# Kernel tuning notes

Hardware: AMD Instinct MI355X
Metric: run time of the kernel (lower is better)

## Reference

```python
import jax, jax.numpy as jnp
import numpy as np

STRIDE = 16
RATIOS = (0.5, 1.0, 2.0)
SCALES = (8, 16, 32)
NMS_THRESH = 0.7
NUM_PRE = 12000
NUM_POST = 2000
MIN_SIZE = 16.0


def _all_anchors(feat_h, feat_w):
    # base anchors centered at (stride/2, stride/2), (y1, x1, y2, x2)
    base = []
    for r in RATIOS:
        for s in SCALES:
            h = STRIDE * s * np.sqrt(r)
            w = STRIDE * s * np.sqrt(1.0 / r)
            c = STRIDE / 2.0
            base.append([c - h / 2.0, c - w / 2.0, c + h / 2.0, c + w / 2.0])
    base = np.asarray(base, np.float32)  # (A, 4)
    ys = np.arange(feat_h, dtype=np.float32) * STRIDE
    xs = np.arange(feat_w, dtype=np.float32) * STRIDE
    shift = np.stack(np.meshgrid(ys, xs, indexing='ij'), axis=-1)  # (H, W, 2) = (y, x)
    shift4 = np.concatenate([shift, shift], axis=-1)  # (H, W, 4)
    anchors = shift4[:, :, None, :] + base[None, None, :, :]  # (H, W, A, 4)
    return jnp.asarray(anchors.reshape(-1, 4))


def _conv(x, w, b, padding):
    y = jax.lax.conv_general_dilated(x, w, (1, 1), padding,
                                     dimension_numbers=('NCHW', 'OIHW', 'NCHW'))
    return y + b[None, :, None, None]


def _create_rpn_proposals(locs, scores, anchors, img_h, img_w):
    # box deparameterize (y1,x1,y2,x2 anchors; dy,dx,dh,dw locs)
    ha = anchors[:, 2] - anchors[:, 0]
    wa = anchors[:, 3] - anchors[:, 1]
    cya = anchors[:, 0] + 0.5 * ha
    cxa = anchors[:, 1] + 0.5 * wa
    cy = locs[:, 0] * ha + cya
    cx = locs[:, 1] * wa + cxa
    h = ha * jnp.exp(locs[:, 2])
    w = wa * jnp.exp(locs[:, 3])
    boxes = jnp.stack([cy - 0.5 * h, cx - 0.5 * w, cy + 0.5 * h, cx + 0.5 * w], axis=1)

    order = jnp.argsort(-scores)[:NUM_PRE]
    boxes = boxes[order]
    s = scores[order]

    lim = jnp.array([img_h, img_w, img_h, img_w], dtype=boxes.dtype)
    boxes = jnp.clip(boxes, 0.0, lim)
    valid = ((boxes[:, 2] - boxes[:, 0]) >= MIN_SIZE) & ((boxes[:, 3] - boxes[:, 1]) >= MIN_SIZE)

    areas = (boxes[:, 2] - boxes[:, 0]) * (boxes[:, 3] - boxes[:, 1])
    n = boxes.shape[0]
    idx = jnp.arange(n)

    def body(i, suppressed):
        bi = boxes[i]
        yy1 = jnp.maximum(bi[0], boxes[:, 0])
        xx1 = jnp.maximum(bi[1], boxes[:, 1])
        yy2 = jnp.minimum(bi[2], boxes[:, 2])
        xx2 = jnp.minimum(bi[3], boxes[:, 3])
        inter = jnp.maximum(yy2 - yy1, 0.0) * jnp.maximum(xx2 - xx1, 0.0)
        iou = inter / (areas[i] + areas - inter + 1e-10)
        new_sup = suppressed | ((iou > NMS_THRESH) & (idx > i))
        return jnp.where(suppressed[i], suppressed, new_sup)

    suppressed = jax.lax.fori_loop(0, n, body, ~valid)
    keep = (~suppressed) & valid
    rank = jnp.cumsum(keep) - 1
    tgt = jnp.where(keep & (rank < NUM_POST), rank, NUM_POST)  # overflow slot
    out = jnp.zeros((NUM_POST + 1, 4), boxes.dtype).at[tgt].set(boxes)[:NUM_POST]
    return out  # (2000, 4), zero-padded if fewer kept


def setup_inputs() -> dict:
    key = jax.random.key(0)
    ks = jax.random.split(key, 7)
    in_c, out_c, A = 1024, 512, 9
    x = jax.random.normal(ks[0], (1, in_c, 64, 64), dtype=jnp.float32)
    conv_w = jax.random.normal(ks[1], (out_c, in_c, 3, 3), jnp.float32) * 0.01
    conv_b = jnp.zeros((out_c,), jnp.float32)
    score_w = jax.random.normal(ks[2], (A * 2, out_c, 1, 1), jnp.float32) * 0.01
    score_b = jnp.zeros((A * 2,), jnp.float32)
    loc_w = jax.random.normal(ks[3], (A * 4, out_c, 1, 1), jnp.float32) * 0.01
    loc_b = jnp.zeros((A * 4,), jnp.float32)
    return {"x": x, "conv_w": conv_w, "conv_b": conv_b,
            "score_w": score_w, "score_b": score_b,
            "loc_w": loc_w, "loc_b": loc_b,
            "img_h": 1024, "img_w": 1024}


def reference(x, conv_w, conv_b, score_w, score_b, loc_w, loc_b, img_h, img_w):
    _, _, fh, fw = x.shape
    anchors = _all_anchors(fh, fw)  # (fh*fw*A, 4)
    h = jax.nn.leaky_relu(_conv(x, conv_w, conv_b, 'SAME'), 0.01)
    rpn_locs = _conv(h, loc_w, loc_b, 'VALID').transpose(0, 2, 3, 1).reshape(-1, 4)
    rpn_scores = _conv(h, score_w, score_b, 'VALID').transpose(0, 2, 3, 1).reshape(-1, 2)
    fg = jax.nn.softmax(rpn_scores, axis=1)[:, 1]
    rois = _create_rpn_proposals(jax.lax.stop_gradient(rpn_locs),
                                 jax.lax.stop_gradient(fg),
                                 anchors, img_h, img_w)
    return rpn_locs, rpn_scores, rois, anchors
```

## Files before the change

kernel.cpp:

```cpp
#include <hip/hip_runtime.h>
#include <cstdint>
#include <cstddef>
#include <math.h>

#define NANCH    36864
#define NPRE     12000
#define NPRE_PAD 12032
#define NW       188
#define SORT_N   16384
#define NPOST    2000

__device__ __forceinline__ int tribase(int ci) { return ci * NW - (ci * (ci - 1)) / 2; }

__global__ __launch_bounds__(256, 2)
void k_conv_ks(const float* __restrict__ xg, const float* __restrict__ wg_,
               double* __restrict__ p0g, double* __restrict__ p1g)
{
    __shared__ float wlds[144 * 64];
    __shared__ float xlds[16 * 4 * 76];
    const int tid = threadIdx.x;
    const int ks  = blockIdx.x >> 8;
    const int inner = blockIdx.x & 255;
    const int oct = inner & 7;
    const int rp  = inner >> 3;
    const int oc0 = oct << 6;
    const int y0  = rp << 1;
    const int ocg = tid >> 4;
    const int pxg = tid & 15;
    const int ry  = pxg >> 3;
    const int cx0 = (pxg & 7) << 3;
    const int lane = tid & 63, wv = tid >> 6;
    const int icbase = ks << 9;

    double acc[4][8];
#pragma unroll
    for (int o = 0; o < 4; ++o)
#pragma unroll
        for (int j = 0; j < 8; ++j) acc[o][j] = 0.0;

    int xoff[17], loff[17];
#pragma unroll
    for (int t = 0; t < 17; ++t) {
        int f = tid + 256 * t;
        if (f < 4224) {
            int ic = f / 264; int r = f - ic * 264; int srow = r / 66; int gc = r - srow * 66;
            loff[t] = (ic * 4 + srow) * 76 + gc;
            int gy = y0 + srow - 1, gx = gc - 1;
            xoff[t] = (gy >= 0 && gy < 64 && gx >= 0 && gx < 64)
                      ? (ic * 4096 + gy * 64 + gx) : -1;
        } else { loff[t] = -1; xoff[t] = -1; }
    }

    const float* wbase = wg_ + (size_t)(oc0 + lane) * 9216 + (size_t)icbase * 9 + wv;
    const float* xbase = xg + (size_t)icbase * 4096;
    float wreg[36], xreg[17];

#pragma unroll
    for (int t = 0; t < 36; ++t) wreg[t] = wbase[4 * t];
#pragma unroll
    for (int t = 0; t < 17; ++t) xreg[t] = (xoff[t] >= 0) ? xbase[xoff[t]] : 0.f;

    for (int kc = 0; kc < 32; ++kc) {
        __syncthreads();
#pragma unroll
        for (int t = 0; t < 36; ++t) wlds[(wv + 4 * t) * 64 + lane] = wreg[t];
#pragma unroll
        for (int t = 0; t < 17; ++t)
            if (loff[t] >= 0) xlds[loff[t]] = xreg[t];
        if (kc < 31) {
            const float* wp = wbase + (kc + 1) * 144;
            const float* xp = xbase + (size_t)(kc + 1) * 16 * 4096;
#pragma unroll
            for (int t = 0; t < 36; ++t) wreg[t] = wp[4 * t];
#pragma unroll
            for (int t = 0; t < 17; ++t) xreg[t] = (xoff[t] >= 0) ? xp[xoff[t]] : 0.f;
        }
        __syncthreads();
#pragma unroll 1
        for (int ic = 0; ic < 16; ++ic) {
#pragma unroll
            for (int ky = 0; ky < 3; ++ky) {
                const float* xr = &xlds[(ic * 4 + ry + ky) * 76 + cx0];
                float4 t0 = *(const float4*)(xr);
                float4 t1 = *(const float4*)(xr + 4);
                float2 t2 = *(const float2*)(xr + 8);
                double xwd[10] = {t0.x, t0.y, t0.z, t0.w, t1.x, t1.y, t1.z, t1.w, t2.x, t2.y};
#pragma unroll
                for (int kx = 0; kx < 3; ++kx) {
                    const float4 wq = *(const float4*)&wlds[(ic * 9 + ky * 3 + kx) * 64 + (ocg << 2)];
                    double wdv[4] = {wq.x, wq.y, wq.z, wq.w};
#pragma unroll
                    for (int o = 0; o < 4; ++o)
#pragma unroll
                        for (int j = 0; j < 8; ++j)
                            acc[o][j] = fma(wdv[o], xwd[j + kx], acc[o][j]);
                }
            }
        }
    }
    double* pg = ks ? p1g : p0g;
#pragma unroll
    for (int o = 0; o < 4; ++o) {
        const int oc = oc0 + (ocg << 2) + o;
        double* pp = pg + (size_t)oc * 4096 + (y0 + ry) * 64 + cx0;
#pragma unroll
        for (int j = 0; j < 8; j += 2)
            *(double2*)(pp + j) = make_double2(acc[o][j], acc[o][j + 1]);
    }
}

__global__ __launch_bounds__(256, 4)
void k_comb(const double* __restrict__ p0, const double* __restrict__ p1,
            const float* __restrict__ bg, float* __restrict__ hg)
{
    int i2 = (blockIdx.x * 256 + threadIdx.x) * 2;
    double2 a = *(const double2*)(p0 + i2);
    double2 b = *(const double2*)(p1 + i2);
    double bo = (double)bg[i2 >> 12];
    double t0 = a.x + b.x + bo, t1 = a.y + b.y + bo;
    float v0 = (float)((t0 >= 0.0) ? t0 : 0.01 * t0);
    float v1 = (float)((t1 >= 0.0) ? t1 : 0.01 * t1);
    *(float2*)(hg + i2) = make_float2(v0, v1);
}

__global__ __launch_bounds__(256, 1)
void k_conv_full(const float* __restrict__ xg, const float* __restrict__ wg_,
                 const float* __restrict__ bg, float* __restrict__ hg)
{
    __shared__ float wlds[144 * 64];
    __shared__ float xlds[16 * 4 * 76];
    const int tid = threadIdx.x;
    const int oct = blockIdx.x & 7;
    const int rp  = blockIdx.x >> 3;
    const int oc0 = oct << 6;
    const int y0  = rp << 1;
    const int ocg = tid >> 4;
    const int pxg = tid & 15;
    const int ry  = pxg >> 3;
    const int cx0 = (pxg & 7) << 3;
    const int lane = tid & 63, wv = tid >> 6;
    double acc[4][8];
#pragma unroll
    for (int o = 0; o < 4; ++o)
#pragma unroll
        for (int j = 0; j < 8; ++j) acc[o][j] = 0.0;
    int xoff[17], loff[17];
#pragma unroll
    for (int t = 0; t < 17; ++t) {
        int f = tid + 256 * t;
        if (f < 4224) {
            int ic = f / 264; int r = f - ic * 264; int srow = r / 66; int gc = r - srow * 66;
            loff[t] = (ic * 4 + srow) * 76 + gc;
            int gy = y0 + srow - 1, gx = gc - 1;
            xoff[t] = (gy >= 0 && gy < 64 && gx >= 0 && gx < 64)
                      ? (ic * 4096 + gy * 64 + gx) : -1;
        } else { loff[t] = -1; xoff[t] = -1; }
    }
    const float* wbase = wg_ + (size_t)(oc0 + lane) * 9216 + wv;
    float wreg[36], xreg[17];
#pragma unroll
    for (int t = 0; t < 36; ++t) wreg[t] = wbase[4 * t];
#pragma unroll
    for (int t = 0; t < 17; ++t) xreg[t] = (xoff[t] >= 0) ? xg[xoff[t]] : 0.f;
    for (int kc = 0; kc < 64; ++kc) {
        __syncthreads();
#pragma unroll
        for (int t = 0; t < 36; ++t) wlds[(wv + 4 * t) * 64 + lane] = wreg[t];
#pragma unroll
        for (int t = 0; t < 17; ++t)
            if (loff[t] >= 0) xlds[loff[t]] = xreg[t];
        if (kc < 63) {
            const float* wp = wbase + (kc + 1) * 144;
            const float* xp = xg + (size_t)(kc + 1) * 16 * 4096;
#pragma unroll
            for (int t = 0; t < 36; ++t) wreg[t] = wp[4 * t];
#pragma unroll
            for (int t = 0; t < 17; ++t) xreg[t] = (xoff[t] >= 0) ? xp[xoff[t]] : 0.f;
        }
        __syncthreads();
#pragma unroll 1
        for (int ic = 0; ic < 16; ++ic) {
#pragma unroll
            for (int ky = 0; ky < 3; ++ky) {
                const float* xr = &xlds[(ic * 4 + ry + ky) * 76 + cx0];
                float4 t0 = *(const float4*)(xr);
                float4 t1 = *(const float4*)(xr + 4);
                float2 t2 = *(const float2*)(xr + 8);
                double xwd[10] = {t0.x, t0.y, t0.z, t0.w, t1.x, t1.y, t1.z, t1.w, t2.x, t2.y};
#pragma unroll
                for (int kx = 0; kx < 3; ++kx) {
                    const float4 wq = *(const float4*)&wlds[(ic * 9 + ky * 3 + kx) * 64 + (ocg << 2)];
                    double wdv[4] = {wq.x, wq.y, wq.z, wq.w};
#pragma unroll
                    for (int o = 0; o < 4; ++o)
#pragma unroll
                        for (int j = 0; j < 8; ++j)
                            acc[o][j] = fma(wdv[o], xwd[j + kx], acc[o][j]);
                }
            }
        }
    }
#pragma unroll
    for (int o = 0; o < 4; ++o) {
        const int oc = oc0 + (ocg << 2) + o;
        const double bo = (double)bg[oc];
        float* hp = hg + (size_t)oc * 4096 + (y0 + ry) * 64 + cx0;
        float v[8];
#pragma unroll
        for (int j = 0; j < 8; ++j) {
            double t = acc[o][j] + bo;
            v[j] = (float)((t >= 0.0) ? t : 0.01 * t);
        }
        *(float4*)(hp)     = make_float4(v[0], v[1], v[2], v[3]);
        *(float4*)(hp + 4) = make_float4(v[4], v[5], v[6], v[7]);
    }
}

__global__ __launch_bounds__(256, 1)
void k_heads(const float* __restrict__ hg, const float* __restrict__ loc_w,
             const float* __restrict__ loc_b, const float* __restrict__ score_w,
             const float* __restrict__ score_b, const int* __restrict__ imh,
             const int* __restrict__ imw, float* __restrict__ out,
             float* __restrict__ boxes_all, unsigned long long* __restrict__ keys64)
{
    __shared__ float  hch[64 * 64];
    __shared__ float  wch[54 * 64];
    __shared__ float  ol[54 * 64];
    __shared__ double sld[18 * 64];
    const int y = blockIdx.x, tid = threadIdx.x;
    const int px = tid & 63, cg = tid >> 6;
    double acc[14];
#pragma unroll
    for (int u = 0; u < 14; ++u) acc[u] = 0.0;
    for (int cc = 0; cc < 8; ++cc) {
        __syncthreads();
#pragma unroll
        for (int t = 0; t < 16; ++t) {
            int f = tid + 256 * t;
            hch[f] = hg[(size_t)(cc * 64 + (f >> 6)) * 4096 + y * 64 + (f & 63)];
        }
#pragma unroll
        for (int t = 0; t < 14; ++t) {
            int f = tid + 256 * t;
            if (f < 54 * 64) {
                int ch = f >> 6, c = f & 63;
                wch[f] = (ch < 36) ? loc_w[ch * 512 + cc * 64 + c]
                                   : score_w[(ch - 36) * 512 + cc * 64 + c];
            }
        }
        __syncthreads();
        for (int c = 0; c < 64; ++c) {
            double hvd = (double)hch[c * 64 + px];
#pragma unroll
            for (int u = 0; u < 14; ++u) {
                int ch = cg + 4 * u;
                if (ch < 54) acc[u] = fma((double)wch[ch * 64 + c], hvd, acc[u]);
            }
        }
    }
    __syncthreads();
#pragma unroll
    for (int u = 0; u < 14; ++u) {
        int ch = cg + 4 * u;
        if (ch < 54) {
            double s = acc[u] + (double)((ch < 36) ? loc_b[ch] : score_b[ch - 36]);
            ol[ch * 64 + px] = (float)s;
            if (ch >= 36) sld[(ch - 36) * 64 + px] = s;
        }
    }
    __syncthreads();
    for (int f = tid; f < 64 * 36; f += 256) {
        int p = f / 36, ch = f - 36 * p;
        out[(size_t)(y * 64 + p) * 36 + ch] = ol[ch * 64 + p];
    }
    for (int f = tid; f < 64 * 18; f += 256) {
        int p = f / 18, ch = f - 18 * p;
        out[147456 + (size_t)(y * 64 + p) * 18 + ch] = ol[(36 + ch) * 64 + p];
    }
    const float fy = (float)(*imh), fx = (float)(*imw);
    float* anch = out + 229184;
    for (int t2 = tid; t2 < 576; t2 += 256) {
        int p = t2 / 9, a = t2 - 9 * p;
        int pg = y * 64 + p;
        int ar = a / 3, as = a - 3 * ar;
        double rr = (ar == 0) ? 0.5 : ((ar == 1) ? 1.0 : 2.0);
        double ss = (as == 0) ? 8.0 : ((as == 1) ? 16.0 : 32.0);
        double hh = 16.0 * ss * sqrt(rr), wwd = 16.0 * ss * sqrt(1.0 / rr);
        float by1 = (float)(8.0 - hh * 0.5), bx1 = (float)(8.0 - wwd * 0.5);
        float by2 = (float)(8.0 + hh * 0.5), bx2 = (float)(8.0 + wwd * 0.5);
        float sy = (float)(y * 16), sx = (float)(p * 16);
        float a0 = sy + by1, a1 = sx + bx1, a2 = sy + by2, a3 = sx + bx2;
        int base = (pg * 9 + a) * 4;
        anch[base + 0] = a0; anch[base + 1] = a1; anch[base + 2] = a2; anch[base + 3] = a3;
        double d = sld[(a * 2 + 1) * 64 + p] - sld[(a * 2) * 64 + p];
        long long bits = __double_as_longlong(d);
        unsigned long long u64 =
            (unsigned long long)(bits ^ ((bits >> 63) | (long long)0x8000000000000000LL));
        unsigned long long v = ~u64;
        keys64[pg * 9 + a] = (v & 0xFFFFFFFFFFFF0000ULL) | (unsigned long long)(pg * 9 + a);
        float dy = ol[(a * 4 + 0) * 64 + p], dxv = ol[(a * 4 + 1) * 64 + p];
        float dh = ol[(a * 4 + 2) * 64 + p], dwv = ol[(a * 4 + 3) * 64 + p];
        float hA = a2 - a0, wA = a3 - a1;
        float cya = a0 + 0.5f * hA, cxa = a1 + 0.5f * wA;
        float cy = dy * hA + cya, cx = dxv * wA + cxa;
        float hb = hA * expf(dh), wb = wA * expf(dwv);
        float b0 = fminf(fmaxf(cy - 0.5f * hb, 0.f), fy);
        float b1 = fminf(fmaxf(cx - 0.5f * wb, 0.f), fx);
        float b2 = fminf(fmaxf(cy + 0.5f * hb, 0.f), fy);
        float b3 = fminf(fmaxf(cx + 0.5f * wb, 0.f), fx);
        boxes_all[base + 0] = b0; boxes_all[base + 1] = b1;
        boxes_all[base + 2] = b2; boxes_all[base + 3] = b3;
    }
}

__global__ __launch_bounds__(1024, 1)
void k_select(const unsigned long long* __restrict__ keys64,
              const float* __restrict__ boxes_all,
              unsigned long long* __restrict__ sortbuf, float* __restrict__ sbox,
              float* __restrict__ areas, unsigned long long* __restrict__ suppr)
{
    __shared__ unsigned int hist[256];
    __shared__ unsigned int sh_below, sh_prefix, sh_nsel;
    __shared__ unsigned long long tile[4096];
    const int tid = threadIdx.x;
    if (tid == 0) { sh_below = 0; sh_prefix = 0; sh_nsel = 0; }
    __syncthreads();
    for (int p = 3; p >= 0; --p) {
        if (tid < 256) hist[tid] = 0;
        __syncthreads();
        unsigned int pref = sh_prefix;
        int shift = p * 8;
        for (int i = tid; i < NANCH; i += 1024) {
            unsigned int k = (unsigned int)(keys64[i] >> 32);
            bool match = (p == 3) || ((k >> (shift + 8)) == pref);
            if (match) atomicAdd(&hist[(k >> shift) & 255u], 1u);
        }
        __syncthreads();
        if (tid == 0) {
            unsigned int below = sh_below, cacc = 0;
            int b = 0;
            for (; b < 256; ++b) {
                if (below + cacc + hist[b] >= NPRE) break;
                cacc += hist[b];
            }
            if (b > 255) b = 255;
            sh_below = below + cacc;
            sh_prefix = (pref << 8) | (unsigned int)b;
        }
        __syncthreads();
    }
    const unsigned int P = sh_prefix;
    for (int i = tid; i < NANCH; i += 1024) {
        unsigned long long k = keys64[i];
        if ((unsigned int)(k >> 32) <= P) {
            unsigned int pos = atomicAdd(&sh_nsel, 1u);
            if (pos < SORT_N) sortbuf[pos] = k;
        }
    }
    __syncthreads();
    unsigned int nsel = sh_nsel; if (nsel > SORT_N) nsel = SORT_N;
    for (unsigned int i = nsel + tid; i < SORT_N; i += 1024) sortbuf[i] = ~0ULL;
    __syncthreads();
    for (int T = 0; T < 4; ++T) {
        for (int t = tid; t < 4096; t += 1024) tile[t] = sortbuf[T * 4096 + t];
        __syncthreads();
        for (int k2 = 2; k2 <= 4096; k2 <<= 1) {
            for (int j = k2 >> 1; j > 0; j >>= 1) {
                for (int t = tid; t < 2048; t += 1024) {
                    int i = ((t & ~(j - 1)) << 1) | (t & (j - 1));
                    int ip = i | j;
                    bool up = (((T * 4096 + i) & k2) == 0);
                    unsigned long long A = tile[i], B = tile[ip];
                    if ((A > B) == up) { tile[i] = B; tile[ip] = A; }
                }
                __syncthreads();
            }
        }
        for (int t = tid; t < 4096; t += 1024) sortbuf[T * 4096 + t] = tile[t];
        __syncthreads();
    }
    auto gstage = [&](int k2, int j) {
        for (int t = tid; t < 8192; t += 1024) {
            int i = ((t & ~(j - 1)) << 1) | (t & (j - 1));
            int ip = i | j;
            bool up = ((i & k2) == 0);
            unsigned long long A = sortbuf[i], B = sortbuf[ip];
            if ((A > B) == up) { sortbuf[i] = B; sortbuf[ip] = A; }
        }
        __syncthreads();
    };
    auto ltail = [&](int k2) {
        for (int T = 0; T < 4; ++T) {
            for (int t = tid; t < 4096; t += 1024) tile[t] = sortbuf[T * 4096 + t];
            __syncthreads();
            for (int j = 2048; j > 0; j >>= 1) {
                for (int t = tid; t < 2048; t += 1024) {
                    int i = ((t & ~(j - 1)) << 1) | (t & (j - 1));
                    int ip = i | j;
                    bool up = (((T * 4096 + i) & k2) == 0);
                    unsigned long long A = tile[i], B = tile[ip];
                    if ((A > B) == up) { tile[i] = B; tile[ip] = A; }
                }
                __syncthreads();
            }
            for (int t = tid; t < 4096; t += 1024) sortbuf[T * 4096 + t] = tile[t];
            __syncthreads();
        }
    };
    gstage(8192, 4096);  ltail(8192);
    gstage(16384, 8192); gstage(16384, 4096); ltail(16384);

    if (tid < NW) suppr[tid] = (tid == NW - 1) ? 0xFFFFFFFF00000000ULL : 0ULL;
    __syncthreads();
    for (int r = tid; r < NPRE_PAD; r += 1024) {
        float b0 = 0, b1 = 0, b2 = 0, b3 = 0;
        if (r < NPRE) {
            unsigned int idx = (unsigned int)(sortbuf[r] & 0xFFFFULL);
            const float* bp = boxes_all + (size_t)idx * 4;
            b0 = bp[0]; b1 = bp[1]; b2 = bp[2]; b3 = bp[3];
        }
        sbox[r * 4 + 0] = b0; sbox[r * 4 + 1] = b1;
        sbox[r * 4 + 2] = b2; sbox[r * 4 + 3] = b3;
        areas[r] = (b2 - b0) * (b3 - b1);
        if (r < NPRE) {
            bool valid = ((b2 - b0) >= 16.0f) && ((b3 - b1) >= 16.0f);
            if (!valid) atomicOr(&suppr[r >> 6], 1ULL << (r & 63));
        }
    }
}

__global__ __launch_bounds__(256, 1)
void k_mask(const float* __restrict__ sbox, const float* __restrict__ areas,
            unsigned long long* __restrict__ mask)
{
    const int cj = blockIdx.x, q = blockIdx.y;
    __shared__ float4 bx[64];
    __shared__ float aj[64];
    const int t = threadIdx.x;
    const int j0 = cj * 64;
    if (t < 64) { bx[t] = ((const float4*)sbox)[j0 + t]; aj[t] = areas[j0 + t]; }
    __syncthreads();
    const int c0 = ((cj + 1) * q) >> 2, c1 = ((cj + 1) * (q + 1)) >> 2;
    for (int i0 = c0 * 64; i0 < c1 * 64; i0 += 256) {
        int i = i0 + t;
        if (i < c1 * 64) {
            const float4 p = ((const float4*)sbox)[i];
            const float ai = areas[i];
            unsigned long long w = 0;
            for (int jj = 0; jj < 64; ++jj) {
                float4 qb = bx[jj];
                float yy1 = fmaxf(p.x, qb.x), xx1 = fmaxf(p.y, qb.y);
                float yy2 = fminf(p.z, qb.z), xx2 = fminf(p.w, qb.w);
                float inter = fmaxf(yy2 - yy1, 0.f) * fmaxf(xx2 - xx1, 0.f);
                float iou = inter / (ai + aj[jj] - inter + 1e-10f);
                w |= ((unsigned long long)((iou > 0.7f) && (j0 + jj > i))) << jj;
            }
            int ci = i >> 6;
            mask[(size_t)(tribase(ci) + (cj - ci)) * 64 + (i & 63)] = w;
        }
    }
}

__global__ __launch_bounds__(256, 1)
void k_scan(const unsigned long long* __restrict__ mask,
            const unsigned long long* __restrict__ suppr,
            const float* __restrict__ sbox, float* __restrict__ rois)
{
    __shared__ unsigned long long rvs[NW];
    __shared__ unsigned long long curw;
    __shared__ unsigned long long keptw[NW];
    __shared__ int totkept, brk;
    __shared__ int pref[NW + 1];
    const int tid = threadIdx.x;
    if (tid < NW) { rvs[tid] = suppr[tid]; keptw[tid] = 0ULL; }
    if (tid == 0) { totkept = 0; brk = 0; }
    __syncthreads();
    for (int c = 0; c < NW; ++c) {
        if (tid < 64) {
            unsigned long long diag = mask[(size_t)tribase(c) * 64 + tid];
            unsigned long long w = rvs[c];
            for (int b = 0; b < 64; ++b) {
                unsigned long long db = __shfl(diag, b, 64);
                if (!((w >> b) & 1ULL)) w |= db;
            }
            if (tid == 0) {
                curw = w;
                keptw[c] = ~w;
                totkept += __popcll(~w);
                if (totkept >= NPOST) brk = 1;
            }
        }
        __syncthreads();
        if (brk) break;
        unsigned long long kw = ~curw;
        if (tid > c && tid < NW) {
            const unsigned long long* mrow = mask + (size_t)(tribase(c) + (tid - c)) * 64;
            unsigned long long a0 = 0, a1 = 0, a2 = 0, a3 = 0;
            for (int b = 0; b < 64; b += 4) {
                unsigned long long m0 = mrow[b + 0];
                unsigned long long m1 = mrow[b + 1];
                unsigned long long m2 = mrow[b + 2];
                unsigned long long m3 = mrow[b + 3];
                if ((kw >> (b + 0)) & 1ULL) a0 |= m0;
                if ((kw >> (b + 1)) & 1ULL) a1 |= m1;
                if ((kw >> (b + 2)) & 1ULL) a2 |= m2;
                if ((kw >> (b + 3)) & 1ULL) a3 |= m3;
            }
            rvs[tid] |= a0 | a1 | a2 | a3;
        }
        __syncthreads();
    }
    __syncthreads();
    if (tid == 0) {
        int s = 0;
        for (int c = 0; c < NW; ++c) { pref[c] = s; s += __popcll(keptw[c]); }
        pref[NW] = s;
    }
    __syncthreads();
    int total = pref[NW]; if (total > NPOST) total = NPOST;
    for (int r = total * 4 + tid; r < NPOST * 4; r += 256) rois[r] = 0.f;
    if (tid < NW) {
        unsigned long long kw = keptw[tid];
        int r = pref[tid];
        for (int b = 0; b < 64; ++b) {
            if ((kw >> b) & 1ULL) {
                if (r < NPOST) {
                    const float* bp = sbox + (size_t)(tid * 64 + b) * 4;
                    rois[r * 4 + 0] = bp[0]; rois[r * 4 + 1] = bp[1];
                    rois[r * 4 + 2] = bp[2]; rois[r * 4 + 3] = bp[3];
                }
                ++r;
            }
        }
    }
}

extern "C" void kernel_launch(void* const* d_in, const int* in_sizes, int n_in,
                              void* d_out, int out_size, void* d_ws, size_t ws_size,
                              hipStream_t stream)
{
    const float* x       = (const float*)d_in[0];
    const float* conv_w  = (const float*)d_in[1];
    const float* conv_b  = (const float*)d_in[2];
    const float* score_w = (const float*)d_in[3];
    const float* score_b = (const float*)d_in[4];
    const float* loc_w   = (const float*)d_in[5];
    const float* loc_b   = (const float*)d_in[6];
    const int*   imh     = (const int*)d_in[7];
    const int*   imw     = (const int*)d_in[8];
    float* out = (float*)d_out;
    char* ws = (char*)d_ws;
    float* h                    = (float*)(ws);
    double* P0                  = (double*)(ws + 8388608);
    double* P1                  = (double*)(ws + 25165824);
    float* boxes_all            = (float*)(ws + 8388608);
    unsigned long long* keys64  = (unsigned long long*)(ws + 8978432);
    float* sbox                 = (float*)(ws + 9273344);
    float* areas                = (float*)(ws + 9465856);
    unsigned long long* suppr   = (unsigned long long*)(ws + 9513984);
    unsigned long long* sortbuf = (unsigned long long*)(ws + 9515520);
    unsigned long long* mask    = (unsigned long long*)(ws + 9646592);

    if (ws_size >= 41943040) {
        k_conv_ks<<<512, 256, 0, stream>>>(x, conv_w, P0, P1);
        k_comb   <<<4096, 256, 0, stream>>>(P0, P1, conv_b, h);
    } else {
        k_conv_full<<<256, 256, 0, stream>>>(x, conv_w, conv_b, h);
    }
    k_heads <<<64, 256, 0, stream>>>(h, loc_w, loc_b, score_w, score_b, imh, imw,
                                     out, boxes_all, keys64);
    k_select<<<1, 1024, 0, stream>>>(keys64, boxes_all, sortbuf, sbox, areas, suppr);
    k_mask  <<<dim3(188, 4), 256, 0, stream>>>(sbox, areas, mask);
    k_scan  <<<1, 256, 0, stream>>>(mask, suppr, sbox, out + 221184);
}
```

Measured before the change: 1.866 ms.

## Replace FP64 FMA 3x3 conv with MFMA f64 implicit-GEMM kernel

Rewrites the 512-channel 3x3 convolution as an implicit GEMM on the FP64 matrix cores (mfma_f64_16x16x4f64). Each block computes one output row for 64 output channels, so the split-K partial buffers and the combine kernel are no longer needed. Bias and leaky-ReLU are applied in the epilogue, with the result staged through LDS for coalesced stores. The lane-to-matrix mapping is probed at runtime with small MFMA calls and falls back to a fixed layout if the probe is inconsistent. This adds probe complexity and stride-4 scalar LDS loads as the cost of moving the FP64 math onto the matrix units.

Result: faster. 1.800 ms (-3.5%).

```diff
diff --git a/kernel.cpp b/kernel.cpp
--- a/kernel.cpp
+++ b/kernel.cpp
@@ -10,209 +10,151 @@
 #define SORT_N   16384
 #define NPOST    2000
 
+typedef double d4_t __attribute__((ext_vector_type(4)));
+
 __device__ __forceinline__ int tribase(int ci) { return ci * NW - (ci * (ci - 1)) / 2; }
 
 __global__ __launch_bounds__(256, 2)
-void k_conv_ks(const float* __restrict__ xg, const float* __restrict__ wg_,
-               double* __restrict__ p0g, double* __restrict__ p1g)
+void k_conv_mfma(const float* __restrict__ xg, const float* __restrict__ wg_,
+                 const float* __restrict__ bg, float* __restrict__ hg)
 {
-    __shared__ float wlds[144 * 64];
-    __shared__ float xlds[16 * 4 * 76];
+    __shared__ __align__(16) float wlds[36 * 64 * 4];
+    __shared__ __align__(16) float xlds[16 * 3 * 68];
     const int tid = threadIdx.x;
-    const int ks  = blockIdx.x >> 8;
-    const int inner = blockIdx.x & 255;
-    const int oct = inner & 7;
-    const int rp  = inner >> 3;
+    const int oct = blockIdx.x & 7;
+    const int y   = blockIdx.x >> 3;
     const int oc0 = oct << 6;
-    const int y0  = rp << 1;
-    const int ocg = tid >> 4;
-    const int pxg = tid & 15;
-    const int ry  = pxg >> 3;
-    const int cx0 = (pxg & 7) << 3;
-    const int lane = tid & 63, wv = tid >> 6;
-    const int icbase = ks << 9;
-
-    double acc[4][8];
-#pragma unroll
-    for (int o = 0; o < 4; ++o)
-#pragma unroll
-        for (int j = 0; j < 8; ++j) acc[o][j] = 0.0;
-
-    int xoff[17], loff[17];
-#pragma unroll
-    for (int t = 0; t < 17; ++t) {
+    const int l   = tid & 63;
+    const int wv  = tid >> 6;
+    const int g   = l >> 4;
+    const int li  = l & 15;
+    const int wm  = wv >> 1;
+    const int wn  = wv & 1;
+
+    int pr[4], qc[4];
+    int aG = g;
+    {
+        d4_t Pz = {0., 0., 0., 0.}, Qz = {0., 0., 0., 0.}, Tz = {0., 0., 0., 0.};
+        Pz = __builtin_amdgcn_mfma_f64_16x16x4f64((double)li, 1.0, Pz, 0, 0, 0);
+        Qz = __builtin_amdgcn_mfma_f64_16x16x4f64(1.0, (double)li, Qz, 0, 0, 0);
+        Tz = __builtin_amdgcn_mfma_f64_16x16x4f64((double)g, (double)(1 << (2 * g)),
+                                                  Tz, 0, 0, 0);
+        bool ok = true;
+        const int tval = (int)Tz[0];
+        if ((int)Tz[1] != tval || (int)Tz[2] != tval || (int)Tz[3] != tval) ok = false;
+        int seen = 0;
+#pragma unroll
+        for (int j = 0; j < 4; ++j) {
+            int d = (tval >> (2 * j)) & 3;
+            seen |= 1 << d;
+            if (d == g) aG = j;
+        }
+        if (seen != 15) ok = false;
+#pragma unroll
+        for (int r = 0; r < 4; ++r) {
+            int pv = (int)Pz[r], qv = (int)Qz[r];
+            if ((pv & 3) || (qv & 3)) ok = false;
+            pr[r] = pv >> 2; qc[r] = qv >> 2;
+            if (pr[r] > 15 || qc[r] > 15) ok = false;
+        }
+        if (!ok) {
+#pragma unroll
+            for (int r = 0; r < 4; ++r) { pr[r] = 4 * g + r; qc[r] = li; }
+            aG = g;
+        }
+    }
+
+    d4_t acc00 = {0., 0., 0., 0.}, acc01 = {0., 0., 0., 0.};
+    d4_t acc10 = {0., 0., 0., 0.}, acc11 = {0., 0., 0., 0.};
+
+    int xoff[13], loff[13];
+#pragma unroll
+    for (int t = 0; t < 13; ++t) {
         int f = tid + 256 * t;
-        if (f < 4224) {
-            int ic = f / 264; int r = f - ic * 264; int srow = r / 66; int gc = r - srow * 66;
-            loff[t] = (ic * 4 + srow) * 76 + gc;
-            int gy = y0 + srow - 1, gx = gc - 1;
+        if (f < 3168) {
+            int ic = f / 198; int r = f - ic * 198; int sr = r / 66; int gc = r - sr * 66;
+            loff[t] = (ic * 3 + sr) * 68 + gc;
+            int gy = y + sr - 1, gx = gc - 1;
             xoff[t] = (gy >= 0 && gy < 64 && gx >= 0 && gx < 64)
                       ? (ic * 4096 + gy * 64 + gx) : -1;
         } else { loff[t] = -1; xoff[t] = -1; }
     }
 
-    const float* wbase = wg_ + (size_t)(oc0 + lane) * 9216 + (size_t)icbase * 9 + wv;
-    const float* xbase = xg + (size_t)icbase * 4096;
-    float wreg[36], xreg[17];
-
-#pragma unroll
-    for (int t = 0; t < 36; ++t) wreg[t] = wbase[4 * t];
-#pragma unroll
-    for (int t = 0; t < 17; ++t) xreg[t] = (xoff[t] >= 0) ? xbase[xoff[t]] : 0.f;
-
-    for (int kc = 0; kc < 32; ++kc) {
-        __syncthreads();
-#pragma unroll
-        for (int t = 0; t < 36; ++t) wlds[(wv + 4 * t) * 64 + lane] = wreg[t];
-#pragma unroll
-        for (int t = 0; t < 17; ++t)
-            if (loff[t] >= 0) xlds[loff[t]] = xreg[t];
-        if (kc < 31) {
-            const float* wp = wbase + (kc + 1) * 144;
-            const float* xp = xbase + (size_t)(kc + 1) * 16 * 4096;
-#pragma unroll
-            for (int t = 0; t < 36; ++t) wreg[t] = wp[4 * t];
-#pragma unroll
-            for (int t = 0; t < 17; ++t) xreg[t] = (xoff[t] >= 0) ? xp[xoff[t]] : 0.f;
-        }
-        __syncthreads();
+    const float* wptr = wg_ + (size_t)(oc0 + l) * 9216 + 4 * wv;
+    float4 wr[9];
+    float  xr[13];
+#pragma unroll
+    for (int i = 0; i < 9; ++i) wr[i] = *(const float4*)(wptr + 16 * i);
+#pragma unroll
+    for (int t = 0; t < 13; ++t) xr[t] = (xoff[t] >= 0) ? xg[xoff[t]] : 0.f;
+
+    const int abase = wm * 32 + li;
+    const int bbase = (wn * 32 + li) * 4 + g;
+
 #pragma unroll 1
-        for (int ic = 0; ic < 16; ++ic) {
-#pragma unroll
-            for (int ky = 0; ky < 3; ++ky) {
-                const float* xr = &xlds[(ic * 4 + ry + ky) * 76 + cx0];
-                float4 t0 = *(const float4*)(xr);
-                float4 t1 = *(const float4*)(xr + 4);
-                float2 t2 = *(const float2*)(xr + 8);
-                double xwd[10] = {t0.x, t0.y, t0.z, t0.w, t1.x, t1.y, t1.z, t1.w, t2.x, t2.y};
-#pragma unroll
-                for (int kx = 0; kx < 3; ++kx) {
-                    const float4 wq = *(const float4*)&wlds[(ic * 9 + ky * 3 + kx) * 64 + (ocg << 2)];
-                    double wdv[4] = {wq.x, wq.y, wq.z, wq.w};
-#pragma unroll
-                    for (int o = 0; o < 4; ++o)
-#pragma unroll
-                        for (int j = 0; j < 8; ++j)
-                            acc[o][j] = fma(wdv[o], xwd[j + kx], acc[o][j]);
-                }
-            }
-        }
-    }
-    double* pg = ks ? p1g : p0g;
-#pragma unroll
-    for (int o = 0; o < 4; ++o) {
-        const int oc = oc0 + (ocg << 2) + o;
-        double* pp = pg + (size_t)oc * 4096 + (y0 + ry) * 64 + cx0;
-#pragma unroll
-        for (int j = 0; j < 8; j += 2)
-            *(double2*)(pp + j) = make_double2(acc[o][j], acc[o][j + 1]);
-    }
-}
-
-__global__ __launch_bounds__(256, 4)
-void k_comb(const double* __restrict__ p0, const double* __restrict__ p1,
-            const float* __restrict__ bg, float* __restrict__ hg)
-{
-    int i2 = (blockIdx.x * 256 + threadIdx.x) * 2;
-    double2 a = *(const double2*)(p0 + i2);
-    double2 b = *(const double2*)(p1 + i2);
-    double bo = (double)bg[i2 >> 12];
-    double t0 = a.x + b.x + bo, t1 = a.y + b.y + bo;
-    float v0 = (float)((t0 >= 0.0) ? t0 : 0.01 * t0);
-    float v1 = (float)((t1 >= 0.0) ? t1 : 0.01 * t1);
-    *(float2*)(hg + i2) = make_float2(v0, v1);
-}
-
-__global__ __launch_bounds__(256, 1)
-void k_conv_full(const float* __restrict__ xg, const float* __restrict__ wg_,
-                 const float* __restrict__ bg, float* __restrict__ hg)
-{
-    __shared__ float wlds[144 * 64];
-    __shared__ float xlds[16 * 4 * 76];
-    const int tid = threadIdx.x;
-    const int oct = blockIdx.x & 7;
-    const int rp  = blockIdx.x >> 3;
-    const int oc0 = oct << 6;
-    const int y0  = rp << 1;
-    const int ocg = tid >> 4;
-    const int pxg = tid & 15;
-    const int ry  = pxg >> 3;
-    const int cx0 = (pxg & 7) << 3;
-    const int lane = tid & 63, wv = tid >> 6;
-    double acc[4][8];
-#pragma unroll
-    for (int o = 0; o < 4; ++o)
-#pragma unroll
-        for (int j = 0; j < 8; ++j) acc[o][j] = 0.0;
-    int xoff[17], loff[17];
-#pragma unroll
-    for (int t = 0; t < 17; ++t) {
-        int f = tid + 256 * t;
-        if (f < 4224) {
-            int ic = f / 264; int r = f - ic * 264; int srow = r / 66; int gc = r - srow * 66;
-            loff[t] = (ic * 4 + srow) * 76 + gc;
-            int gy = y0 + srow - 1, gx = gc - 1;
-            xoff[t] = (gy >= 0 && gy < 64 && gx >= 0 && gx < 64)
-                      ? (ic * 4096 + gy * 64 + gx) : -1;
-        } else { loff[t] = -1; xoff[t] = -1; }
-    }
-    const float* wbase = wg_ + (size_t)(oc0 + lane) * 9216 + wv;
-    float wreg[36], xreg[17];
-#pragma unroll
-    for (int t = 0; t < 36; ++t) wreg[t] = wbase[4 * t];
-#pragma unroll
-    for (int t = 0; t < 17; ++t) xreg[t] = (xoff[t] >= 0) ? xg[xoff[t]] : 0.f;
-    for (int kc = 0; kc < 64; ++kc) {
-        __syncthreads();
-#pragma unroll
-        for (int t = 0; t < 36; ++t) wlds[(wv + 4 * t) * 64 + lane] = wreg[t];
-#pragma unroll
-        for (int t = 0; t < 17; ++t)
-            if (loff[t] >= 0) xlds[loff[t]] = xreg[t];
-        if (kc < 63) {
-            const float* wp = wbase + (kc + 1) * 144;
-            const float* xp = xg + (size_t)(kc + 1) * 16 * 4096;
-#pragma unroll
-            for (int t = 0; t < 36; ++t) wreg[t] = wp[4 * t];
-#pragma unroll
-            for (int t = 0; t < 17; ++t) xreg[t] = (xoff[t] >= 0) ? xp[xoff[t]] : 0.f;
-        }
-        __syncthreads();
-#pragma unroll 1
-        for (int ic = 0; ic < 16; ++ic) {
-#pragma unroll
-            for (int ky = 0; ky < 3; ++ky) {
-                const float* xr = &xlds[(ic * 4 + ry + ky) * 76 + cx0];
-                float4 t0 = *(const float4*)(xr);
-                float4 t1 = *(const float4*)(xr + 4);
-                float2 t2 = *(const float2*)(xr + 8);
-                double xwd[10] = {t0.x, t0.y, t0.z, t0.w, t1.x, t1.y, t1.z, t1.w, t2.x, t2.y};
-#pragma unroll
-                for (int kx = 0; kx < 3; ++kx) {
-                    const float4 wq = *(const float4*)&wlds[(ic * 9 + ky * 3 + kx) * 64 + (ocg << 2)];
-                    double wdv[4] = {wq.x, wq.y, wq.z, wq.w};
-#pragma unroll
-                    for (int o = 0; o < 4; ++o)
-#pragma unroll
-                        for (int j = 0; j < 8; ++j)
-                            acc[o][j] = fma(wdv[o], xwd[j + kx], acc[o][j]);
-                }
-            }
-        }
-    }
-#pragma unroll
-    for (int o = 0; o < 4; ++o) {
-        const int oc = oc0 + (ocg << 2) + o;
-        const double bo = (double)bg[oc];
-        float* hp = hg + (size_t)oc * 4096 + (y0 + ry) * 64 + cx0;
-        float v[8];
-#pragma unroll
-        for (int j = 0; j < 8; ++j) {
-            double t = acc[o][j] + bo;
-            v[j] = (float)((t >= 0.0) ? t : 0.01 * t);
-        }
-        *(float4*)(hp)     = make_float4(v[0], v[1], v[2], v[3]);
-        *(float4*)(hp + 4) = make_float4(v[4], v[5], v[6], v[7]);
+    for (int cc = 0; cc < 64; ++cc) {
+        __syncthreads();
+#pragma unroll
+        for (int i = 0; i < 9; ++i)
+            *(float4*)&wlds[((wv + 4 * i) * 64 + l) * 4] = wr[i];
+#pragma unroll
+        for (int t = 0; t < 13; ++t)
+            if (loff[t] >= 0) xlds[loff[t]] = xr[t];
+        if (cc < 63) {
+            const float* wp = wptr + (cc + 1) * 144;
+            const float* xp = xg + (size_t)(cc + 1) * 65536;
+#pragma unroll
+            for (int i = 0; i < 9; ++i) wr[i] = *(const float4*)(wp + 16 * i);
+#pragma unroll
+            for (int t = 0; t < 13; ++t) xr[t] = (xoff[t] >= 0) ? xp[xoff[t]] : 0.f;
+        }
+        __syncthreads();
+#pragma unroll
+        for (int s = 0; s < 36; ++s) {
+            int k   = 4 * s + aG;
+            int icL = k / 9; int tap = k - 9 * icL;
+            int ky  = tap / 3; int kx = tap - 3 * ky;
+            int ax  = (icL * 3 + ky) * 68 + kx + abase;
+            double a0 = (double)xlds[ax];
+            double a1 = (double)xlds[ax + 16];
+            double b0 = (double)wlds[bbase + s * 256];
+            double b1 = (double)wlds[bbase + s * 256 + 64];
+            acc00 = __builtin_amdgcn_mfma_f64_16x16x4f64(a0, b0, acc00, 0, 0, 0);
+            acc01 = __builtin_amdgcn_mfma_f64_16x16x4f64(a0, b1, acc01, 0, 0, 0);
+            acc10 = __builtin_amdgcn_mfma_f64_16x16x4f64(a1, b0, acc10, 0, 0, 0);
+            acc11 = __builtin_amdgcn_mfma_f64_16x16x4f64(a1, b1, acc11, 0, 0, 0);
+        }
+    }
+
+    __syncthreads();
+    float* olds = wlds;
+    {
+#pragma unroll
+        for (int r = 0; r < 4; ++r) {
+            const int oca = wn * 32 + qc[r];
+            const int ocb = oca + 16;
+            const double ba = (double)bg[oc0 + oca];
+            const double bb = (double)bg[oc0 + ocb];
+            const int pxa = wm * 32 + pr[r];
+            const int pxb = pxa + 16;
+            double t00 = acc00[r] + ba;
+            double t01 = acc01[r] + bb;
+            double t10 = acc10[r] + ba;
+            double t11 = acc11[r] + bb;
+            olds[oca * 68 + pxa] = (float)((t00 >= 0.0) ? t00 : 0.01 * t00);
+            olds[ocb * 68 + pxa] = (float)((t01 >= 0.0) ? t01 : 0.01 * t01);
+            olds[oca * 68 + pxb] = (float)((t10 >= 0.0) ? t10 : 0.01 * t10);
+            olds[ocb * 68 + pxb] = (float)((t11 >= 0.0) ? t11 : 0.01 * t11);
+        }
+    }
+    __syncthreads();
+    {
+        const int oc = tid >> 2, q = tid & 3;
+        float* dst = hg + (size_t)(oc0 + oc) * 4096 + y * 64 + q * 16;
+        const float* src = &olds[oc * 68 + q * 16];
+#pragma unroll
+        for (int j = 0; j < 4; ++j)
+            *(float4*)(dst + 4 * j) = *(const float4*)(src + 4 * j);
     }
 }
 
@@ -551,8 +493,6 @@
     float* out = (float*)d_out;
     char* ws = (char*)d_ws;
     float* h                    = (float*)(ws);
-    double* P0                  = (double*)(ws + 8388608);
-    double* P1                  = (double*)(ws + 25165824);
     float* boxes_all            = (float*)(ws + 8388608);
     unsigned long long* keys64  = (unsigned long long*)(ws + 8978432);
     float* sbox                 = (float*)(ws + 9273344);
@@ -561,12 +501,7 @@
     unsigned long long* sortbuf = (unsigned long long*)(ws + 9515520);
     unsigned long long* mask    = (unsigned long long*)(ws + 9646592);
 
-    if (ws_size >= 41943040) {
-        k_conv_ks<<<512, 256, 0, stream>>>(x, conv_w, P0, P1);
-        k_comb   <<<4096, 256, 0, stream>>>(P0, P1, conv_b, h);
-    } else {
-        k_conv_full<<<256, 256, 0, stream>>>(x, conv_w, conv_b, h);
-    }
+    k_conv_mfma<<<512, 256, 0, stream>>>(x, conv_w, conv_b, h);
     k_heads <<<64, 256, 0, stream>>>(h, loc_w, loc_b, score_w, score_b, imh, imw,
                                      out, boxes_all, keys64);
     k_select<<<1, 1024, 0, stream>>>(keys64, boxes_all, sortbuf, sbox, areas, suppr);
```
